# Kernel tuning notes

Hardware: AMD Instinct MI355X
Metric: run time of the kernel (lower is better)

## Reference

```python
import jax, jax.numpy as jnp
import numpy as np

N_QUBITS = 8
N_LAYERS = 3
BN_EPS = 1e-5


def _apply_ry(state, theta, wire):
    # state: (B, 2, ..., 2) real statevector; theta: scalar or (B,)
    st = jnp.moveaxis(state, wire + 1, 1)
    t = jnp.asarray(theta, state.dtype)
    t = t.reshape(t.shape + (1,) * (state.ndim - 2))  # broadcast vs (B, 2^{n-1})
    c, s = jnp.cos(t / 2), jnp.sin(t / 2)
    s0, s1 = st[:, 0], st[:, 1]
    new = jnp.stack([c * s0 - s * s1, s * s0 + c * s1], axis=1)
    return jnp.moveaxis(new, 1, wire + 1)


def _apply_cnot(state, ctrl, tgt):
    # assumes ctrl < tgt (chain topology used by the circuit)
    st = jnp.moveaxis(state, ctrl + 1, 1)
    a0, a1 = st[:, 0], st[:, 1]
    a1 = jnp.flip(a1, axis=tgt)  # target axis is tgt after removing the ctrl axis
    new = jnp.stack([a0, a1], axis=1)
    return jnp.moveaxis(new, 1, ctrl + 1)


def _circuit(enc_angles, params):
    # Batched 8-qubit statevector simulation; RY/CNOT are real so the state is real.
    B = enc_angles.shape[0]
    state = jnp.zeros((B, 2 ** N_QUBITS), enc_angles.dtype).at[:, 0].set(1.0)
    state = state.reshape((B,) + (2,) * N_QUBITS)
    for i in range(4):  # feature-map encoder on first 4 wires
        state = _apply_ry(state, enc_angles[:, i], i)
    for layer in range(N_LAYERS):
        for q in range(N_QUBITS):
            state = _apply_ry(state, params[layer, q], q)
        for q in range(N_QUBITS - 1):
            state = _apply_cnot(state, q, q + 1)
    probs = state * state
    ez = []
    for w in range(N_QUBITS):
        axes = tuple(a for a in range(1, N_QUBITS + 1) if a != w + 1)
        p = probs.sum(axis=axes)  # (B, 2)
        ez.append(p[:, 0] - p[:, 1])  # <Z_w>
    return jnp.stack(ez, axis=-1)  # (B, N_QUBITS)


def setup_inputs() -> dict:
    key = jax.random.key(0)
    k1, k2, k3, k4 = jax.random.split(key, 4)
    B = 65536
    return {
        "x": jax.random.normal(k1, (B, 1, 12, 12), dtype=jnp.float32),
        "params": jax.random.normal(k2, (N_LAYERS, N_QUBITS), dtype=jnp.float32),
        "W": jax.random.normal(k3, (4, N_QUBITS), dtype=jnp.float32) * 0.3,
        "b": jax.random.normal(k4, (4,), dtype=jnp.float32) * 0.1,
        "gamma": jnp.ones((4,), dtype=jnp.float32),
        "beta": jnp.zeros((4,), dtype=jnp.float32),
    }


def reference(x, params, W, b, gamma, beta):
    B = x.shape[0]
    # avg_pool2d(kernel_size=6) on 12x12 -> 2x2, then flatten to 4 encoding angles
    pooled = x.reshape(B, 1, 2, 6, 2, 6).mean(axis=(3, 5)).reshape(B, 4)
    q_out = _circuit(pooled, params)          # (B, 8)
    out = q_out @ W.T + b                      # Linear(8 -> 4)
    mean = out.mean(axis=0)                    # BatchNorm1d training mode
    var = out.var(axis=0)                      # biased variance (torch BN)
    return gamma * (out - mean) / jnp.sqrt(var + BN_EPS) + beta
```

## Files before the change

kernel.cpp:

```cpp
#include <hip/hip_runtime.h>
#include <math.h>

#define NQ 8
#define NS 256
#define NK 16
#define NL 3
#define XS 20
#define MTS 260

__global__ __launch_bounds__(256) void setup_kernel(
    const float* __restrict__ params,
    const float* __restrict__ W,
    float* __restrict__ R_ws,
    double* __restrict__ acc)
{
    __shared__ float X[NS * XS];
    __shared__ float MT[NK * MTS];
    __shared__ float PT[NK * MTS];
    const int t = threadIdx.x;
    const int j = blockIdx.x;

    if (j == 0) acc[t] = 0.0;

    float m[NK];
    #pragma unroll
    for (int k = 0; k < NK; ++k) m[k] = 0.f;
    if ((t & 15) == 0) m[t >> 4] = 1.f;

    for (int layer = 0; layer < NL; ++layer) {
        for (int q = 0; q < NQ; ++q) {
            const float th = params[layer * 8 + q] * 0.5f;
            const float c  = __cosf(th);
            const float sn = __sinf(th);
            const int mask = 1 << (7 - q);
            const float ss = (t & mask) ? sn : -sn;
            float p[NK];
            if (mask >= 64) {
                __syncthreads();
                #pragma unroll
                for (int k = 0; k < NK; k += 4)
                    *(float4*)&X[t * XS + k] = make_float4(m[k], m[k+1], m[k+2], m[k+3]);
                __syncthreads();
                const int pt = t ^ mask;
                #pragma unroll
                for (int k = 0; k < NK; k += 4) {
                    float4 v = *(const float4*)&X[pt * XS + k];
                    p[k] = v.x; p[k+1] = v.y; p[k+2] = v.z; p[k+3] = v.w;
                }
            } else {
                #pragma unroll
                for (int k = 0; k < NK; ++k) p[k] = __shfl_xor(m[k], mask);
            }
            #pragma unroll
            for (int k = 0; k < NK; ++k) m[k] = fmaf(ss, p[k], c * m[k]);
        }
        int src = t;
        #pragma unroll
        for (int q = 6; q >= 0; --q) {
            int bit = (src >> (7 - q)) & 1;
            src ^= bit << (6 - q);
        }
        __syncthreads();
        #pragma unroll
        for (int k = 0; k < NK; k += 4)
            *(float4*)&X[t * XS + k] = make_float4(m[k], m[k+1], m[k+2], m[k+3]);
        __syncthreads();
        #pragma unroll
        for (int k = 0; k < NK; k += 4) {
            float4 v = *(const float4*)&X[src * XS + k];
            m[k] = v.x; m[k+1] = v.y; m[k+2] = v.z; m[k+3] = v.w;
        }
    }

    float ts = 0.f;
    #pragma unroll
    for (int w = 0; w < 8; ++w) {
        float sign = ((t >> (7 - w)) & 1) ? -1.f : 1.f;
        ts += W[j * 8 + w] * sign;
    }

    #pragma unroll
    for (int k = 0; k < NK; ++k) {
        MT[k * MTS + t] = m[k];
        PT[k * MTS + t] = ts * m[k];
    }
    __syncthreads();

    const int k = t >> 4, l = t & 15;
    const float4* mk4 = (const float4*)&MT[k * MTS];
    const float4* pl4 = (const float4*)&PT[l * MTS];
    float r = 0.f;
    #pragma unroll 8
    for (int i = 0; i < NS / 4; ++i) {
        float4 a = mk4[i];
        float4 b = pl4[i];
        r = fmaf(a.x, b.x, r);
        r = fmaf(a.y, b.y, r);
        r = fmaf(a.z, b.z, r);
        r = fmaf(a.w, b.w, r);
    }
    R_ws[j * 256 + t] = r;
}

__global__ __launch_bounds__(256, 4) void main_kernel(
    const float* __restrict__ x,
    const float* __restrict__ bvec,
    const float* __restrict__ R_ws,
    float* __restrict__ out_col,
    double* __restrict__ acc,
    int B)
{
    __shared__ float4 tile[2304];
    __shared__ float  part[64 * 9];

    const int t   = threadIdx.x;
    const int blk = blockIdx.x;

    const float4* xg = (const float4*)x + (size_t)blk * 2304;
    #pragma unroll
    for (int i = 0; i < 9; ++i) tile[i * 256 + t] = xg[i * 256 + t];
    __syncthreads();

    {
        float sl = 0.f, sr = 0.f;
        #pragma unroll
        for (int i = 0; i < 9; ++i) {
            float4 v = tile[t * 9 + i];
            const int mod = i % 3;
            if (mod == 0)      { sl += v.x + v.y + v.z + v.w; }
            else if (mod == 1) { sl += v.x + v.y; sr += v.z + v.w; }
            else               { sr += v.x + v.y + v.z + v.w; }
        }
        part[(t >> 2) * 9 + (t & 3) * 2 + 0] = sl;
        part[(t >> 2) * 9 + (t & 3) * 2 + 1] = sr;
    }
    __syncthreads();

    const int e = t & 63;
    const int p = __builtin_amdgcn_readfirstlane(t >> 6);

    const float* pe = &part[e * 9];
    const float k36 = 0.5f / 36.f;
    float th0 = (pe[0] + pe[2]) * k36;
    float th1 = (pe[1] + pe[3]) * k36;
    float th2 = (pe[4] + pe[6]) * k36;
    float th3 = (pe[5] + pe[7]) * k36;

    float c0 = __cosf(th0), s0 = __sinf(th0);
    float c1 = __cosf(th1), s1 = __sinf(th1);
    float c2 = __cosf(th2), s2 = __sinf(th2);
    float c3 = __cosf(th3), s3 = __sinf(th3);

    float u[4] = { c0 * c1, c0 * s1, s0 * c1, s0 * s1 };
    float v[4] = { c2 * c3, c2 * s3, s2 * c3, s2 * s3 };
    float a[16];
    #pragma unroll
    for (int i = 0; i < 4; ++i)
        #pragma unroll
        for (int jj = 0; jj < 4; ++jj) a[i * 4 + jj] = u[i] * v[jj];

    const float* Rp = R_ws + p * 256;
    float o = bvec[p];
    #pragma unroll
    for (int kk = 0; kk < 16; ++kk) {
        float dot = 0.f;
        #pragma unroll
        for (int ll = 0; ll < 16; ++ll) dot = fmaf(Rp[kk * 16 + ll], a[ll], dot);
        o = fmaf(a[kk], dot, o);
    }

    out_col[(size_t)p * B + blk * 64 + e] = o;

    float s1v = o, s2v = o * o;
    #pragma unroll
    for (int off = 1; off < 64; off <<= 1) {
        s1v += __shfl_xor(s1v, off);
        s2v += __shfl_xor(s2v, off);
    }
    if (e == 0) {
        const int bin = blk & 31;
        atomicAdd(&acc[bin * 8 + p],     (double)s1v);
        atomicAdd(&acc[bin * 8 + 4 + p], (double)s2v);
    }
}

__global__ __launch_bounds__(256) void bn_kernel(
    const float* __restrict__ out_col,
    const double* __restrict__ acc,
    const float* __restrict__ gamma,
    const float* __restrict__ beta,
    float* __restrict__ outp,
    int B)
{
    __shared__ float sc[4], sh[4];
    const int t = threadIdx.x;
    if (t < 4) {
        double s = 0.0, s2 = 0.0;
        #pragma unroll
        for (int bin = 0; bin < 32; ++bin) {
            s  += acc[bin * 8 + t];
            s2 += acc[bin * 8 + 4 + t];
        }
        double invB = 1.0 / (double)B;
        double mean = s * invB;
        double var  = s2 * invB - mean * mean;
        float inv   = (float)(1.0 / sqrt(var + 1e-5));
        float g     = gamma[t] * inv;
        sc[t] = g;
        sh[t] = beta[t] - (float)mean * g;
    }
    __syncthreads();

    const int i = blockIdx.x * 256 + t;
    float o0 = out_col[(size_t)0 * B + i];
    float o1 = out_col[(size_t)1 * B + i];
    float o2 = out_col[(size_t)2 * B + i];
    float o3 = out_col[(size_t)3 * B + i];
    float4 r;
    r.x = fmaf(o0, sc[0], sh[0]);
    r.y = fmaf(o1, sc[1], sh[1]);
    r.z = fmaf(o2, sc[2], sh[2]);
    r.w = fmaf(o3, sc[3], sh[3]);
    ((float4*)outp)[i] = r;
}

extern "C" void kernel_launch(void* const* d_in, const int* in_sizes, int n_in,
                              void* d_out, int out_size, void* d_ws, size_t ws_size,
                              hipStream_t stream)
{
    const float* x      = (const float*)d_in[0];
    const float* params = (const float*)d_in[1];
    const float* W      = (const float*)d_in[2];
    const float* bvec   = (const float*)d_in[3];
    const float* gamma  = (const float*)d_in[4];
    const float* beta   = (const float*)d_in[5];

    const int B = in_sizes[0] / 144;

    float*  R_ws    = (float*)d_ws;
    double* acc     = (double*)((char*)d_ws + 4096);
    float*  out_col = (float*)((char*)d_ws + 8192);

    float* outp = (float*)d_out;

    setup_kernel<<<4, 256, 0, stream>>>(params, W, R_ws, acc);
    main_kernel<<<B / 64, 256, 0, stream>>>(x, bvec, R_ws, out_col, acc, B);
    bn_kernel<<<B / 256, 256, 0, stream>>>(out_col, acc, gamma, beta, outp, B);
}
```

Baseline: 103.9 us.

## Restructure setup kernel: closed-form first layer, fused CNOT permutation, split-K reduction

Rewrites the small setup kernel that builds the 16x16 quadratic-form matrices. The first layer's RY gates are computed in closed form on the basis state. The CNOT chain permutation is folded into a Gray-code index, and the two high-qubit RYs are merged into a single LDS gather, which removes several barriers. The final 256-length dot products are split across the 4 wavefronts with 2x2 register blocking and then summed through shared memory. Only the tiny 4-block setup kernel changes, so its effect on total time is bounded by how much of the total it takes.

```diff
diff --git a/kernel.cpp b/kernel.cpp
--- a/kernel.cpp
+++ b/kernel.cpp
@@ -22,84 +22,131 @@
 
     if (j == 0) acc[t] = 0.0;
 
+    float cs[NL * NQ], sn[NL * NQ];
+    #pragma unroll
+    for (int i = 0; i < NL * NQ; ++i) {
+        float th = params[i] * 0.5f;
+        cs[i] = __cosf(th);
+        sn[i] = __sinf(th);
+    }
+
     float m[NK];
-    #pragma unroll
-    for (int k = 0; k < NK; ++k) m[k] = 0.f;
-    if ((t & 15) == 0) m[t >> 4] = 1.f;
-
-    for (int layer = 0; layer < NL; ++layer) {
-        for (int q = 0; q < NQ; ++q) {
-            const float th = params[layer * 8 + q] * 0.5f;
-            const float c  = __cosf(th);
-            const float sn = __sinf(th);
-            const int mask = 1 << (7 - q);
-            const float ss = (t & mask) ? sn : -sn;
-            float p[NK];
-            if (mask >= 64) {
-                __syncthreads();
-                #pragma unroll
-                for (int k = 0; k < NK; k += 4)
-                    *(float4*)&X[t * XS + k] = make_float4(m[k], m[k+1], m[k+2], m[k+3]);
-                __syncthreads();
-                const int pt = t ^ mask;
-                #pragma unroll
-                for (int k = 0; k < NK; k += 4) {
-                    float4 v = *(const float4*)&X[pt * XS + k];
-                    p[k] = v.x; p[k+1] = v.y; p[k+2] = v.z; p[k+3] = v.w;
-                }
-            } else {
-                #pragma unroll
-                for (int k = 0; k < NK; ++k) p[k] = __shfl_xor(m[k], mask);
+    {
+        float h = 1.f;
+        #pragma unroll
+        for (int q = 4; q < 8; ++q) {
+            int z = (t >> (7 - q)) & 1;
+            h *= z ? sn[q] : cs[q];
+        }
+        float v[4][2];
+        #pragma unroll
+        for (int q = 0; q < 4; ++q) {
+            int z = (t >> (7 - q)) & 1;
+            v[q][0] = z ? sn[q] : cs[q];
+            v[q][1] = z ? cs[q] : -sn[q];
+        }
+        float p01[4], p23[4];
+        #pragma unroll
+        for (int b0 = 0; b0 < 2; ++b0)
+            #pragma unroll
+            for (int b1 = 0; b1 < 2; ++b1) {
+                p01[b0 * 2 + b1] = v[0][b0] * v[1][b1];
+                p23[b0 * 2 + b1] = v[2][b0] * v[3][b1];
             }
-            #pragma unroll
-            for (int k = 0; k < NK; ++k) m[k] = fmaf(ss, p[k], c * m[k]);
-        }
-        int src = t;
-        #pragma unroll
-        for (int q = 6; q >= 0; --q) {
-            int bit = (src >> (7 - q)) & 1;
-            src ^= bit << (6 - q);
-        }
-        __syncthreads();
+        #pragma unroll
+        for (int k = 0; k < NK; ++k)
+            m[k] = h * p01[k >> 2] * p23[k & 3];
+    }
+
+    #pragma unroll
+    for (int ly = 1; ly < NL; ++ly) {
+        if (ly > 1) __syncthreads();
         #pragma unroll
         for (int k = 0; k < NK; k += 4)
             *(float4*)&X[t * XS + k] = make_float4(m[k], m[k+1], m[k+2], m[k+3]);
         __syncthreads();
-        #pragma unroll
-        for (int k = 0; k < NK; k += 4) {
-            float4 v = *(const float4*)&X[src * XS + k];
-            m[k] = v.x; m[k+1] = v.y; m[k+2] = v.z; m[k+3] = v.w;
-        }
-    }
+
+        const int low = t & 63;
+        float st[4][NK];
+        #pragma unroll
+        for (int i = 0; i < 2; ++i)
+            #pragma unroll
+            for (int jj = 0; jj < 2; ++jj) {
+                int y  = (i << 7) | (jj << 6) | low;
+                int sy = y ^ (y >> 1);
+                #pragma unroll
+                for (int k = 0; k < NK; k += 4) {
+                    float4 vv = *(const float4*)&X[sy * XS + k];
+                    st[i*2+jj][k]   = vv.x; st[i*2+jj][k+1] = vv.y;
+                    st[i*2+jj][k+2] = vv.z; st[i*2+jj][k+3] = vv.w;
+                }
+            }
+
+        const int z7 = (t >> 7) & 1, z6 = (t >> 6) & 1;
+        const float c0 = cs[ly*8+0], s0 = sn[ly*8+0];
+        const float c1 = cs[ly*8+1], s1 = sn[ly*8+1];
+        float u0[2], u1[2];
+        u0[0] = z7 ? s0 : c0;   u0[1] = z7 ? c0 : -s0;
+        u1[0] = z6 ? s1 : c1;   u1[1] = z6 ? c1 : -s1;
+        const float w00 = u0[0]*u1[0], w01 = u0[0]*u1[1];
+        const float w10 = u0[1]*u1[0], w11 = u0[1]*u1[1];
+        #pragma unroll
+        for (int k = 0; k < NK; ++k)
+            m[k] = w00*st[0][k] + w01*st[1][k] + w10*st[2][k] + w11*st[3][k];
+
+        #pragma unroll
+        for (int q = 2; q < NQ; ++q) {
+            const float c = cs[ly*8+q], s = sn[ly*8+q];
+            const int mask = 1 << (7 - q);
+            const float ss = (t & mask) ? s : -s;
+            #pragma unroll
+            for (int k = 0; k < NK; ++k) {
+                float p = __shfl_xor(m[k], mask);
+                m[k] = fmaf(ss, p, c * m[k]);
+            }
+        }
+    }
+
+    int d = t;
+    d ^= d >> 1; d ^= d >> 2; d ^= d >> 4;
 
     float ts = 0.f;
     #pragma unroll
     for (int w = 0; w < 8; ++w) {
-        float sign = ((t >> (7 - w)) & 1) ? -1.f : 1.f;
+        float sign = ((d >> (7 - w)) & 1) ? -1.f : 1.f;
         ts += W[j * 8 + w] * sign;
     }
-
     #pragma unroll
     for (int k = 0; k < NK; ++k) {
-        MT[k * MTS + t] = m[k];
-        PT[k * MTS + t] = ts * m[k];
-    }
-    __syncthreads();
-
-    const int k = t >> 4, l = t & 15;
-    const float4* mk4 = (const float4*)&MT[k * MTS];
-    const float4* pl4 = (const float4*)&PT[l * MTS];
-    float r = 0.f;
-    #pragma unroll 8
-    for (int i = 0; i < NS / 4; ++i) {
-        float4 a = mk4[i];
-        float4 b = pl4[i];
-        r = fmaf(a.x, b.x, r);
-        r = fmaf(a.y, b.y, r);
-        r = fmaf(a.z, b.z, r);
-        r = fmaf(a.w, b.w, r);
-    }
-    R_ws[j * 256 + t] = r;
+        MT[k * MTS + d] = m[k];
+        PT[k * MTS + d] = ts * m[k];
+    }
+    __syncthreads();
+
+    {
+        const int w  = t >> 6;
+        const int ln = t & 63;
+        const int kk = ln >> 3, ll = ln & 7;
+        const float4* A0 = (const float4*)&MT[(2*kk)     * MTS] + w * 16;
+        const float4* A1 = (const float4*)&MT[(2*kk + 1) * MTS] + w * 16;
+        const float4* B0 = (const float4*)&PT[(2*ll)     * MTS] + w * 16;
+        const float4* B1 = (const float4*)&PT[(2*ll + 1) * MTS] + w * 16;
+        float r00 = 0.f, r01 = 0.f, r10 = 0.f, r11 = 0.f;
+        #pragma unroll
+        for (int i = 0; i < 16; ++i) {
+            float4 a0 = A0[i], a1 = A1[i], b0 = B0[i], b1 = B1[i];
+            r00 = fmaf(a0.x,b0.x, fmaf(a0.y,b0.y, fmaf(a0.z,b0.z, fmaf(a0.w,b0.w, r00))));
+            r01 = fmaf(a0.x,b1.x, fmaf(a0.y,b1.y, fmaf(a0.z,b1.z, fmaf(a0.w,b1.w, r01))));
+            r10 = fmaf(a1.x,b0.x, fmaf(a1.y,b0.y, fmaf(a1.z,b0.z, fmaf(a1.w,b0.w, r10))));
+            r11 = fmaf(a1.x,b1.x, fmaf(a1.y,b1.y, fmaf(a1.z,b1.z, fmaf(a1.w,b1.w, r11))));
+        }
+        X[w * 256 + (2*kk)    *16 + 2*ll]     = r00;
+        X[w * 256 + (2*kk)    *16 + 2*ll + 1] = r01;
+        X[w * 256 + (2*kk + 1)*16 + 2*ll]     = r10;
+        X[w * 256 + (2*kk + 1)*16 + 2*ll + 1] = r11;
+        __syncthreads();
+        R_ws[j * 256 + t] = X[t] + X[256 + t] + X[512 + t] + X[768 + t];
+    }
 }
 
 __global__ __launch_bounds__(256, 4) void main_kernel(
```

Result: faster. 101.7 us, median of 2 (-2.0%).
